# Performance work log

Measured on AMD Instinct MI355X. Metric: run time of the kernel, lower is better.

## Reference

```python
import jax, jax.numpy as jnp
import numpy as np
from jax import lax

B, T, N, C, AD, HW, KS, KT = 32, 8, 196, 768, 192, 14, 3, 3
EPS = 1e-5

def _groupnorm1(x, gamma, beta, axes):
    # GroupNorm(1, C): normalize over channel+spatial dims per sample
    mu = jnp.mean(x, axis=axes, keepdims=True)
    var = jnp.mean((x - mu) ** 2, axis=axes, keepdims=True)
    xn = (x - mu) * lax.rsqrt(var + EPS)
    shape = [1] * x.ndim
    shape[1] = -1
    return xn * gamma.reshape(shape) + beta.reshape(shape)

def setup_inputs() -> dict:
    key = jax.random.key(0)
    ks = jax.random.split(key, 16)
    s = 0.02
    return {
        'x': jax.random.normal(ks[0], (B, T, N + 1, C), jnp.float32),
        'w_down': jax.random.normal(ks[1], (C, AD), jnp.float32) * s,
        'b_down': jnp.zeros((AD,), jnp.float32),
        'w_sdw': jax.random.normal(ks[2], (AD, 1, KS, KS), jnp.float32) * s,
        'w_spw': jax.random.normal(ks[3], (AD, AD), jnp.float32) * s,  # [out,in]
        'g_snorm': jnp.ones((AD,), jnp.float32),
        'b_snorm': jnp.zeros((AD,), jnp.float32),
        'w_diff': jax.random.normal(ks[4], (AD, AD), jnp.float32) * s,  # [in,out]
        'w_tdw': jax.random.normal(ks[5], (AD, 1, KT), jnp.float32) * s,
        'w_tpw': jax.random.normal(ks[6], (AD, AD), jnp.float32) * s,  # [out,in]
        'g_tnorm': jnp.ones((AD,), jnp.float32),
        'b_tnorm': jnp.zeros((AD,), jnp.float32),
        'w_g1': jax.random.normal(ks[7], (AD, AD), jnp.float32) * s,
        'b_g1': jnp.zeros((AD,), jnp.float32),
        'w_g2': jax.random.normal(ks[8], (AD, AD), jnp.float32) * s,
        'b_g2': jnp.zeros((AD,), jnp.float32),
        'w_up': jax.random.normal(ks[9], (AD, C), jnp.float32) * s,  # torch zero-inits; randomized for nontrivial test
        'b_up': jnp.zeros((C,), jnp.float32),
        'w_cls': jax.random.normal(ks[10], (AD, C), jnp.float32) * s,
        'b_cls': jnp.zeros((C,), jnp.float32),
    }

def reference(x, w_down, b_down, w_sdw, w_spw, g_snorm, b_snorm, w_diff,
              w_tdw, w_tpw, g_tnorm, b_tnorm, w_g1, b_g1, w_g2, b_g2,
              w_up, b_up, w_cls, b_cls):
    gelu = lambda v: jax.nn.gelu(v, approximate=False)  # torch nn.GELU default (erf)
    cls_token = x[:, :, :1, :]
    patch = x[:, :, 1:, :]
    b, t, n, _ = patch.shape
    hw = HW
    ph = patch @ w_down + b_down  # [b,t,n,ad]
    ad = ph.shape[-1]
    # spatial path: (b t) c h w
    sp = ph.reshape(b * t, hw, hw, ad).transpose(0, 3, 1, 2)
    sp = lax.conv_general_dilated(sp, w_sdw, (1, 1), 'SAME',
                                  feature_group_count=ad,
                                  dimension_numbers=('NCHW', 'OIHW', 'NCHW'))
    sp = _groupnorm1(sp, g_snorm, b_snorm, axes=(1, 2, 3))
    sp = gelu(sp)
    sp = jnp.einsum('bchw,oc->bohw', sp, w_spw)
    spatial = sp.transpose(0, 2, 3, 1).reshape(b, t, n, ad)
    # diff gating
    diff = jnp.concatenate([jnp.zeros_like(ph[:, :1]), ph[:, 1:] - ph[:, :-1]], axis=1)
    diff = diff + diff @ w_diff
    # temporal path: (b n) c t
    tp = (ph + diff).transpose(0, 2, 3, 1).reshape(b * n, ad, t)
    tp = lax.conv_general_dilated(tp, w_tdw, (1,), 'SAME',
                                  feature_group_count=ad,
                                  dimension_numbers=('NCH', 'OIH', 'NCH'))
    tp = _groupnorm1(tp, g_tnorm, b_tnorm, axes=(1, 2))
    tp = gelu(tp)
    tp = jnp.einsum('bct,oc->bot', tp, w_tpw)
    temporal = tp.reshape(b, n, ad, t).transpose(0, 3, 1, 2)
    # gate
    gi = jnp.mean(jnp.abs(diff), axis=(1, 2))  # [b, ad]
    gate = jax.nn.sigmoid(gelu(gi @ w_g1 + b_g1) @ w_g2 + b_g2)[:, None, None, :]
    fused = gate * temporal + (1.0 - gate) * spatial
    patch_out = patch + fused @ w_up + b_up
    cls_ctx = jnp.mean(fused, axis=2, keepdims=True)
    cls_out = cls_token + cls_ctx @ w_cls + b_cls
    return jnp.concatenate([cls_out, patch_out], axis=2)
```

## Files before the change

### kernel.cpp

```cpp
#include <hip/hip_runtime.h>
#include <hip/hip_bf16.h>
#include <math.h>

typedef __attribute__((ext_vector_type(8))) short s8v;
typedef __attribute__((ext_vector_type(4))) float f4v;

#define GN_EPS 1e-5f

__device__ __forceinline__ float s2f(short s) {
    unsigned int u = ((unsigned int)(unsigned short)s) << 16;
    float f; __builtin_memcpy(&f, &u, 4); return f;
}
__device__ __forceinline__ short f2s(float f) {
    __hip_bfloat16 h = __float2bfloat16(f);
    short s; __builtin_memcpy(&s, &h, 2); return s;
}
__device__ __forceinline__ float gelu_f(float x) {
    return 0.5f * x * (1.0f + erff(x * 0.7071067811865476f));
}
__device__ __forceinline__ void gload16(const void* g, void* l) {
    __builtin_amdgcn_global_load_lds((const __attribute__((address_space(1))) void*)g,
                                     (__attribute__((address_space(3))) void*)l,
                                     16, 0, 0);
}

__global__ void detect_kernel(const unsigned int* g_snorm_raw, int* flag) {
    if (threadIdx.x == 0) flag[0] = (g_snorm_raw[0] == 0x3F800000u) ? 1 : 0;
}

struct ConvArgs {
    const void* src[19];
    int cum[20];
};
__global__ __launch_bounds__(256)
void convert_kernel(ConvArgs a, short* __restrict__ dst, const int* __restrict__ dflag,
                    int total) {
    const int dt = dflag[0];
    int idx = blockIdx.x * 256 + threadIdx.x;
    const int stride = gridDim.x * 256;
    for (; idx < total; idx += stride) {
        int seg = 0;
        while (idx >= a.cum[seg + 1]) seg++;
        const int off = idx - a.cum[seg];
        const float v = dt ? ((const float*)a.src[seg])[off]
                           : s2f(((const short*)a.src[seg])[off]);
        dst[idx] = f2s(v);
    }
}

__global__ __launch_bounds__(256)
void transpose_kernel(const short* __restrict__ src, short* __restrict__ dst,
                      int R, int C) {
    const int idx = blockIdx.x * 256 + threadIdx.x;
    if (idx < R * C) {
        const int r = idx / C, c = idx - r * C;
        dst[c * R + r] = src[idx];
    }
}


#define AMAP_PLAIN 0
#define AMAP_X     1
#define AMAP_DIFF  2
#define EPI_BIASH 0
#define EPI_H     1
#define EPI_DIFF  2
#define EPI_UP    3

template<int K_DIM, int N_DIM, int AMAP, int EPI>
__global__ __launch_bounds__(256)
void gemm_kernel(const void* __restrict__ Asrc, const short* __restrict__ Bmat,
                 const short* __restrict__ bias, const short* __restrict__ phH,
                 const void* __restrict__ xExt, short* __restrict__ outH,
                 void* __restrict__ outExt, const int* __restrict__ dflag)
{
    const int dt = dflag[0];

    __shared__ short As[2][2048];
    __shared__ short Bs[2][2048];

    const int tid  = threadIdx.x;
    const int lane = tid & 63;
    const int wave = tid >> 6;
    const int wr = wave >> 1, wc = wave & 1;
    const int m16 = lane & 15, q = lane >> 4;
    const int rowBase = blockIdx.x * 64;
    const int colBase = blockIdx.y * 64;

    const int sr = tid >> 2;
    const int ss = tid & 3;
    const int sg = ss ^ ((sr >> 1) & 3);
    const int wOff = wave * 512;

    const int agrow = rowBase + sr;
    long aBase;
    int abt7 = 0;
    if constexpr (AMAP == AMAP_X) {
        const int bt = agrow / 196;
        aBase = (long)(agrow + bt + 1) * 768 + sg * 8;
    } else if constexpr (AMAP == AMAP_DIFF) {
        aBase = (long)agrow * K_DIM + sg * 8;
        abt7 = (agrow / 196) & 7;
    } else {
        aBase = (long)agrow * K_DIM + sg * 8;
    }
    const long bBase = (long)(colBase + sr) * K_DIM + sg * 8;

    const int ra = wr * 32 + m16;
    const int rb = wc * 32 + m16;
    const int oA0 = ra * 32 + (q ^ ((ra >> 1) & 3)) * 8;
    const int oB0 = rb * 32 + (q ^ ((rb >> 1) & 3)) * 8;
    const int oA1 = oA0 + 512;
    const int oB1 = oB0 + 512;

    f4v acc[2][2] = {};
    constexpr int NK = K_DIM / 32;

    auto stage = [&](int kk, int buf) {
        if constexpr (AMAP == AMAP_PLAIN) {
            gload16((const short*)Asrc + aBase + kk, (void*)&As[buf][wOff]);
        } else if constexpr (AMAP == AMAP_X) {
            if (dt) {
                const float* xp = (const float*)Asrc + aBase + kk;
                const float4 f0 = *(const float4*)xp;
                const float4 f1 = *(const float4*)(xp + 4);
                s8v av;
                av[0] = f2s(f0.x); av[1] = f2s(f0.y); av[2] = f2s(f0.z); av[3] = f2s(f0.w);
                av[4] = f2s(f1.x); av[5] = f2s(f1.y); av[6] = f2s(f1.z); av[7] = f2s(f1.w);
                *(s8v*)&As[buf][sr * 32 + ss * 8] = av;
            } else {
                gload16((const short*)Asrc + aBase + kk, (void*)&As[buf][wOff]);
            }
        } else {
            s8v av;
            if (abt7) {
                const short* p1 = (const short*)Asrc + aBase + kk;
                const s8v v1 = *(const s8v*)p1;
                const s8v v0 = *(const s8v*)(p1 - 37632);
                #pragma unroll
                for (int j = 0; j < 8; j++) av[j] = f2s(s2f(v1[j]) - s2f(v0[j]));
            } else {
                #pragma unroll
                for (int j = 0; j < 8; j++) av[j] = 0;
            }
            *(s8v*)&As[buf][sr * 32 + ss * 8] = av;
        }
        gload16(Bmat + bBase + kk, (void*)&Bs[buf][wOff]);
    };

    stage(0, 0);
    __syncthreads();

    int cur = 0;
    for (int t = 0; t < NK; ++t) {
        if (t + 1 < NK) stage((t + 1) * 32, cur ^ 1);

        const s8v afr0 = *(const s8v*)&As[cur][oA0];
        const s8v afr1 = *(const s8v*)&As[cur][oA1];
        const s8v bfr0 = *(const s8v*)&Bs[cur][oB0];
        const s8v bfr1 = *(const s8v*)&Bs[cur][oB1];

        acc[0][0] = __builtin_amdgcn_mfma_f32_16x16x32_bf16(afr0, bfr0, acc[0][0], 0, 0, 0);
        acc[0][1] = __builtin_amdgcn_mfma_f32_16x16x32_bf16(afr0, bfr1, acc[0][1], 0, 0, 0);
        acc[1][0] = __builtin_amdgcn_mfma_f32_16x16x32_bf16(afr1, bfr0, acc[1][0], 0, 0, 0);
        acc[1][1] = __builtin_amdgcn_mfma_f32_16x16x32_bf16(afr1, bfr1, acc[1][1], 0, 0, 0);

        __syncthreads();
        cur ^= 1;
    }

    #pragma unroll
    for (int i = 0; i < 2; i++) {
        #pragma unroll
        for (int r = 0; r < 4; r++) {
            const int grow = rowBase + wr * 32 + i * 16 + q * 4 + r;
            #pragma unroll
            for (int j = 0; j < 2; j++) {
                const int gc = colBase + wc * 32 + j * 16 + m16;
                float v = acc[i][j][r];
                if constexpr (EPI == EPI_BIASH) {
                    outH[(long)grow * N_DIM + gc] = f2s(v + s2f(bias[gc]));
                } else if constexpr (EPI == EPI_H) {
                    outH[(long)grow * N_DIM + gc] = f2s(v);
                } else if constexpr (EPI == EPI_DIFF) {
                    const int bt = grow / 196;
                    const int t = bt & 7;
                    const float phv = s2f(phH[(long)grow * 192 + gc]);
                    float d = (t > 0) ? (phv - s2f(phH[(long)(grow - 196) * 192 + gc])) : 0.0f;
                    outH[(long)grow * 192 + gc] = f2s(v + phv + d);
                } else {
                    const int bt = grow / 196;
                    const long oi = (long)(grow + bt + 1) * 768 + gc;
                    const float bv = v + s2f(bias[gc]);
                    if (dt) {
                        ((float*)outExt)[oi] = ((const float*)xExt)[oi] + bv;
                    } else {
                        ((short*)outExt)[oi] = f2s(s2f(((const short*)xExt)[oi]) + bv);
                    }
                }
            }
        }
    }
}

__global__ __launch_bounds__(1024, 4)
void spatial_kernel(const short* __restrict__ ph, const short* __restrict__ w_sdw,
                    const short* __restrict__ g_s, const short* __restrict__ b_s,
                    short* __restrict__ snorm)
{
    __shared__ short tile[196 * 192];
    __shared__ short wkT[9 * 192];
    __shared__ float gsl[192], bsl[192];
    __shared__ float redA[16], redB[16];
    __shared__ float stats[2];

    const int bt = blockIdx.x, tid = threadIdx.x;
    const short* Pg = ph + (long)bt * 37632;

    for (int i = tid; i < 4704; i += 1024)
        *(s8v*)&tile[i * 8] = *(const s8v*)&Pg[i * 8];
    for (int i = tid; i < 1728; i += 1024) {
        const int c = i / 9, tap = i - c * 9;
        wkT[tap * 192 + c] = w_sdw[i];
    }
    if (tid < 192) { gsl[tid] = s2f(g_s[tid]); bsl[tid] = s2f(b_s[tid]); }
    __syncthreads();

    float val[5][8];
    float lsum = 0.f, lsq = 0.f;
    #pragma unroll
    for (int it = 0; it < 5; it++) {
        const int i = tid + it * 1024;
        #pragma unroll
        for (int k = 0; k < 8; k++) val[it][k] = 0.f;
        if (i < 4704) {
            const int n = i / 24, c8 = i - n * 24;
            const int h = n / 14, w = n - (n / 14) * 14;
            float a[8] = {0.f,0.f,0.f,0.f,0.f,0.f,0.f,0.f};
            #pragma unroll
            for (int tap = 0; tap < 9; tap++) {
                const int dh = tap / 3 - 1, dw = tap % 3 - 1;
                const int hh = h + dh, ww = w + dw;
                if (hh >= 0 && hh < 14 && ww >= 0 && ww < 14) {
                    s8v iv = *(const s8v*)&tile[(hh * 14 + ww) * 192 + c8 * 8];
                    s8v wv = *(const s8v*)&wkT[tap * 192 + c8 * 8];
                    #pragma unroll
                    for (int k = 0; k < 8; k++) a[k] += s2f(iv[k]) * s2f(wv[k]);
                }
            }
            #pragma unroll
            for (int k = 0; k < 8; k++) {
                val[it][k] = a[k]; lsum += a[k]; lsq += a[k] * a[k];
            }
        }
    }
    #pragma unroll
    for (int d = 1; d < 64; d <<= 1) {
        lsum += __shfl_xor(lsum, d, 64);
        lsq  += __shfl_xor(lsq,  d, 64);
    }
    if ((tid & 63) == 0) { redA[tid >> 6] = lsum; redB[tid >> 6] = lsq; }
    __syncthreads();
    if (tid < 64) {
        float s = (tid < 16) ? redA[tid] : 0.f;
        float qq = (tid < 16) ? redB[tid] : 0.f;
        #pragma unroll
        for (int d = 1; d < 16; d <<= 1) {
            s  += __shfl_xor(s,  d, 64);
            qq += __shfl_xor(qq, d, 64);
        }
        if (tid == 0) {
            const float inv = 1.0f / 37632.0f;
            const float mean = s * inv;
            const float var  = qq * inv - mean * mean;
            stats[0] = mean; stats[1] = rsqrtf(var + GN_EPS);
        }
    }
    __syncthreads();
    const float mean = stats[0], rstd = stats[1];
    short* Og = snorm + (long)bt * 37632;
    #pragma unroll
    for (int it = 0; it < 5; it++) {
        const int i = tid + it * 1024;
        if (i < 4704) {
            const int c8 = i - (i / 24) * 24;
            s8v o;
            #pragma unroll
            for (int k = 0; k < 8; k++) {
                const int c = c8 * 8 + k;
                const float y = (val[it][k] - mean) * rstd * gsl[c] + bsl[c];
                o[k] = f2s(gelu_f(y));
            }
            *(s8v*)&Og[i * 8] = o;
        }
    }
}

__global__ __launch_bounds__(192)
void gi_kernel(const short* __restrict__ tp, const short* __restrict__ ph,
               float* __restrict__ gi)
{
    const int bt = blockIdx.x;
    const int b = bt >> 3;
    const int tid = threadIdx.x;
    const int c8 = tid >> 3, sub = tid & 7;
    float part[8] = {0.f,0.f,0.f,0.f,0.f,0.f,0.f,0.f};
    for (int n = sub; n < 196; n += 8) {
        const long off = ((long)bt * 196 + n) * 192 + c8 * 8;
        s8v a = *(const s8v*)(tp + off);
        s8v p = *(const s8v*)(ph + off);
        #pragma unroll
        for (int k = 0; k < 8; k++) part[k] += fabsf(s2f(a[k]) - s2f(p[k]));
    }
    #pragma unroll
    for (int d = 1; d < 8; d <<= 1) {
        #pragma unroll
        for (int k = 0; k < 8; k++) part[k] += __shfl_xor(part[k], d, 64);
    }
    if (sub == 0) {
        #pragma unroll
        for (int k = 0; k < 8; k++) atomicAdd(&gi[b * 192 + c8 * 8 + k], part[k]);
    }
}

__global__ __launch_bounds__(192)
void temporal_kernel(const short* __restrict__ tp, const short* __restrict__ w_tdw,
                     const short* __restrict__ g_t, const short* __restrict__ b_t,
                     short* __restrict__ tnorm)
{
    const int bn = blockIdx.x;
    const int c = threadIdx.x;
    const int b = bn / 196, n = bn - (bn / 196) * 196;
    const long base = ((long)b * 8 * 196 + n) * 192 + c;
    const long ts = 196 * 192;
    float v[8], o[8];
    #pragma unroll
    for (int t = 0; t < 8; t++) v[t] = s2f(tp[base + t * ts]);
    const float w0 = s2f(w_tdw[c * 3]), w1 = s2f(w_tdw[c * 3 + 1]), w2 = s2f(w_tdw[c * 3 + 2]);
    #pragma unroll
    for (int t = 0; t < 8; t++) {
        float a = v[t] * w1;
        if (t > 0) a += v[t - 1] * w0;
        if (t < 7) a += v[t + 1] * w2;
        o[t] = a;
    }
    float lsum = 0.f, lsq = 0.f;
    #pragma unroll
    for (int t = 0; t < 8; t++) { lsum += o[t]; lsq += o[t] * o[t]; }
    __shared__ float red1[192], red2[192];
    red1[c] = lsum; red2[c] = lsq;
    __syncthreads();
    for (int s = 96; s > 2; s >>= 1) {
        if (c < s) { red1[c] += red1[c + s]; red2[c] += red2[c + s]; }
        __syncthreads();
    }
    const float mean = (red1[0] + red1[1] + red1[2]) * (1.0f / 1536.0f);
    const float var  = (red2[0] + red2[1] + red2[2]) * (1.0f / 1536.0f) - mean * mean;
    const float rstd = rsqrtf(var + GN_EPS);
    const float gg = s2f(g_t[c]), bb = s2f(b_t[c]);
    #pragma unroll
    for (int t = 0; t < 8; t++) {
        const float y = (o[t] - mean) * rstd * gg + bb;
        tnorm[base + t * ts] = f2s(gelu_f(y));
    }
}

__global__ __launch_bounds__(192)
void gate_kernel(const float* __restrict__ gi, const short* __restrict__ w_g1,
                 const short* __restrict__ b_g1, const short* __restrict__ w_g2,
                 const short* __restrict__ b_g2, float* __restrict__ gate)
{
    const int b = blockIdx.x, o = threadIdx.x;
    __shared__ float s0[192], s1[192];
    s0[o] = gi[b * 192 + o] * (1.0f / 1568.0f);
    __syncthreads();
    float a = s2f(b_g1[o]);
    for (int cc = 0; cc < 192; cc++) a += s0[cc] * s2f(w_g1[cc * 192 + o]);
    s1[o] = gelu_f(a);
    __syncthreads();
    float a2 = s2f(b_g2[o]);
    for (int cc = 0; cc < 192; cc++) a2 += s1[cc] * s2f(w_g2[cc * 192 + o]);
    gate[b * 192 + o] = 1.0f / (1.0f + expf(-a2));
}

__global__ __launch_bounds__(192)
void fuse_kernel(const short* __restrict__ temporal, const short* __restrict__ spatial,
                 const float* __restrict__ gate, short* __restrict__ fused,
                 float* __restrict__ cls_sum)
{
    const int bt = blockIdx.x;
    const int b = bt >> 3;
    const int tid = threadIdx.x;
    const int c8 = tid >> 3, sub = tid & 7;
    float g[8];
    {
        const float4* gp = (const float4*)&gate[b * 192 + c8 * 8];
        float4 ga = gp[0], gb = gp[1];
        g[0]=ga.x; g[1]=ga.y; g[2]=ga.z; g[3]=ga.w;
        g[4]=gb.x; g[5]=gb.y; g[6]=gb.z; g[7]=gb.w;
    }
    float part[8] = {0.f,0.f,0.f,0.f,0.f,0.f,0.f,0.f};
    for (int n = sub; n < 196; n += 8) {
        const long off = ((long)bt * 196 + n) * 192 + c8 * 8;
        s8v tv = *(const s8v*)(temporal + off);
        s8v sv = *(const s8v*)(spatial + off);
        s8v fv;
        #pragma unroll
        for (int k = 0; k < 8; k++) {
            const float f = g[k] * s2f(tv[k]) + (1.0f - g[k]) * s2f(sv[k]);
            fv[k] = f2s(f);
            part[k] += f;
        }
        *(s8v*)(fused + off) = fv;
    }
    #pragma unroll
    for (int d = 1; d < 8; d <<= 1) {
        #pragma unroll
        for (int k = 0; k < 8; k++) part[k] += __shfl_xor(part[k], d, 64);
    }
    if (sub == 0) {
        #pragma unroll
        for (int k = 0; k < 8; k++)
            cls_sum[bt * 192 + c8 * 8 + k] = part[k] * (1.0f / 196.0f);
    }
}

__global__ __launch_bounds__(256)
void cls_kernel(const float* __restrict__ cls_sum, const short* __restrict__ w_cls,
                const short* __restrict__ b_cls, const void* __restrict__ x,
                void* __restrict__ out, const int* __restrict__ dflag)
{
    const int dt = dflag[0];
    const int bt = blockIdx.x, tid = threadIdx.x;
    __shared__ float ctx[192];
    if (tid < 192) ctx[tid] = cls_sum[bt * 192 + tid];
    __syncthreads();
    for (int oc = tid; oc < 768; oc += 256) {
        float a = s2f(b_cls[oc]);
        for (int cc = 0; cc < 192; cc++) a += ctx[cc] * s2f(w_cls[cc * 768 + oc]);
        const long oi = (long)bt * 197 * 768 + oc;
        if (dt) ((float*)out)[oi] = ((const float*)x)[oi] + a;
        else    ((short*)out)[oi] = f2s(s2f(((const short*)x)[oi]) + a);
    }
}

extern "C" void kernel_launch(void* const* d_in, const int* in_sizes, int n_in,
                              void* d_out, int out_size, void* d_ws, size_t ws_size,
                              hipStream_t stream) {
    const void* x = d_in[0];

    const long F = 50176L * 192L;
    short* wsS = (short*)d_ws;
    short* P = wsS;
    short* Q = wsS + F;
    short* R = wsS + 2 * F;
    short* S = wsS + 3 * F;
    short* W = wsS + 4 * F;
    int cum[20]; cum[0] = 0;
    for (int i = 1; i <= 19; i++) cum[i] = cum[i - 1] + in_sizes[i];
    const int totalW = cum[19];

    short* WT   = W + ((totalW + 7) & ~7);
    short* wdT  = WT;
    short* wdfT = WT + 147456;
    short* wupT = WT + 147456 + 36864;

    float* smalls = (float*)(WT + 331776);
    float* gi      = smalls;
    float* gate    = smalls + 6144;
    float* cls_sum = smalls + 12288;
    int*   dflag   = (int*)(smalls + 61440);

    const short* b_down = W + cum[1];
    const short* w_sdw  = W + cum[2];
    const short* w_spw  = W + cum[3];
    const short* g_sn   = W + cum[4];
    const short* b_sn   = W + cum[5];
    const short* w_tdw  = W + cum[7];
    const short* w_tpw  = W + cum[8];
    const short* g_tn   = W + cum[9];
    const short* b_tn   = W + cum[10];
    const short* w_g1   = W + cum[11];
    const short* b_g1   = W + cum[12];
    const short* w_g2   = W + cum[13];
    const short* b_g2   = W + cum[14];
    const short* b_up   = W + cum[16];
    const short* w_cls  = W + cum[17];
    const short* b_cls  = W + cum[18];

    hipMemsetAsync(gi, 0, 6144 * sizeof(float), stream);
    detect_kernel<<<1, 64, 0, stream>>>((const unsigned int*)d_in[5], dflag);

    ConvArgs ca;
    for (int i = 0; i < 19; i++) ca.src[i] = d_in[i + 1];
    for (int i = 0; i < 20; i++) ca.cum[i] = cum[i];
    convert_kernel<<<618, 256, 0, stream>>>(ca, W, dflag, totalW);

    transpose_kernel<<<576, 256, 0, stream>>>(W + cum[0],  wdT,  768, 192);
    transpose_kernel<<<144, 256, 0, stream>>>(W + cum[6],  wdfT, 192, 192);
    transpose_kernel<<<576, 256, 0, stream>>>(W + cum[15], wupT, 192, 768);

    dim3 g3(784, 3), g12(784, 12);

    gemm_kernel<768, 192, AMAP_X, EPI_BIASH>
        <<<g3, 256, 0, stream>>>(x, wdT, b_down, nullptr, nullptr, P, nullptr, dflag);
    spatial_kernel<<<256, 1024, 0, stream>>>(P, w_sdw, g_sn, b_sn, R);
    gemm_kernel<192, 192, AMAP_PLAIN, EPI_H>
        <<<g3, 256, 0, stream>>>(R, w_spw, nullptr, nullptr, nullptr, S, nullptr, dflag);
    gemm_kernel<192, 192, AMAP_DIFF, EPI_DIFF>
        <<<g3, 256, 0, stream>>>(P, wdfT, nullptr, P, nullptr, Q, nullptr, dflag);
    gi_kernel<<<256, 192, 0, stream>>>(Q, P, gi);
    temporal_kernel<<<6272, 192, 0, stream>>>(Q, w_tdw, g_tn, b_tn, R);
    gemm_kernel<192, 192, AMAP_PLAIN, EPI_H>
        <<<g3, 256, 0, stream>>>(R, w_tpw, nullptr, nullptr, nullptr, Q, nullptr, dflag);
    gate_kernel<<<32, 192, 0, stream>>>(gi, w_g1, b_g1, w_g2, b_g2, gate);
    fuse_kernel<<<256, 192, 0, stream>>>(Q, S, gate, R, cls_sum);
    gemm_kernel<192, 768, AMAP_PLAIN, EPI_UP>
        <<<g12, 256, 0, stream>>>(R, wupT, b_up, nullptr, x, nullptr, d_out, dflag);
    cls_kernel<<<256, 256, 0, stream>>>(cls_sum, w_cls, b_cls, x, d_out, dflag);
}
```

Measured before the change: 607.4 us.

## Transpose MFMA output for vectorized epilogue stores and fuse gate-input reduction into diff GEMM

Swaps the MFMA operand order so each lane holds four consecutive columns of one row. This lets every GEMM epilogue use 4-wide vector loads and stores instead of scalar ones. The diff GEMM epilogue now also computes |diff| and reduces it across rows with shuffles before atomically adding into the gate input. This removes the separate gi_kernel pass that reread Q and P. The trade-offs are extra shuffle and atomic work inside the GEMM epilogue, and the abs values now come from fp32 before bf16 rounding.

```diff
diff --git a/kernel.cpp b/kernel.cpp
--- a/kernel.cpp
+++ b/kernel.cpp
@@ -3,6 +3,7 @@
 #include <math.h>
 
 typedef __attribute__((ext_vector_type(8))) short s8v;
+typedef __attribute__((ext_vector_type(4))) short s4v;
 typedef __attribute__((ext_vector_type(4))) float f4v;
 
 #define GN_EPS 1e-5f
@@ -72,7 +73,8 @@
 void gemm_kernel(const void* __restrict__ Asrc, const short* __restrict__ Bmat,
                  const short* __restrict__ bias, const short* __restrict__ phH,
                  const void* __restrict__ xExt, short* __restrict__ outH,
-                 void* __restrict__ outExt, const int* __restrict__ dflag)
+                 void* __restrict__ outExt, float* __restrict__ giOut,
+                 const int* __restrict__ dflag)
 {
     const int dt = dflag[0];
 
@@ -160,10 +162,10 @@
         const s8v bfr0 = *(const s8v*)&Bs[cur][oB0];
         const s8v bfr1 = *(const s8v*)&Bs[cur][oB1];
 
-        acc[0][0] = __builtin_amdgcn_mfma_f32_16x16x32_bf16(afr0, bfr0, acc[0][0], 0, 0, 0);
-        acc[0][1] = __builtin_amdgcn_mfma_f32_16x16x32_bf16(afr0, bfr1, acc[0][1], 0, 0, 0);
-        acc[1][0] = __builtin_amdgcn_mfma_f32_16x16x32_bf16(afr1, bfr0, acc[1][0], 0, 0, 0);
-        acc[1][1] = __builtin_amdgcn_mfma_f32_16x16x32_bf16(afr1, bfr1, acc[1][1], 0, 0, 0);
+        acc[0][0] = __builtin_amdgcn_mfma_f32_16x16x32_bf16(bfr0, afr0, acc[0][0], 0, 0, 0);
+        acc[0][1] = __builtin_amdgcn_mfma_f32_16x16x32_bf16(bfr1, afr0, acc[0][1], 0, 0, 0);
+        acc[1][0] = __builtin_amdgcn_mfma_f32_16x16x32_bf16(bfr0, afr1, acc[1][0], 0, 0, 0);
+        acc[1][1] = __builtin_amdgcn_mfma_f32_16x16x32_bf16(bfr1, afr1, acc[1][1], 0, 0, 0);
 
         __syncthreads();
         cur ^= 1;
@@ -171,32 +173,84 @@
 
     #pragma unroll
     for (int i = 0; i < 2; i++) {
-        #pragma unroll
-        for (int r = 0; r < 4; r++) {
-            const int grow = rowBase + wr * 32 + i * 16 + q * 4 + r;
+        const int grow = rowBase + wr * 32 + i * 16 + m16;
+        const int gcb  = colBase + wc * 32 + q * 4;
+
+        if constexpr (EPI == EPI_BIASH) {
             #pragma unroll
             for (int j = 0; j < 2; j++) {
-                const int gc = colBase + wc * 32 + j * 16 + m16;
-                float v = acc[i][j][r];
-                if constexpr (EPI == EPI_BIASH) {
-                    outH[(long)grow * N_DIM + gc] = f2s(v + s2f(bias[gc]));
-                } else if constexpr (EPI == EPI_H) {
-                    outH[(long)grow * N_DIM + gc] = f2s(v);
-                } else if constexpr (EPI == EPI_DIFF) {
-                    const int bt = grow / 196;
-                    const int t = bt & 7;
-                    const float phv = s2f(phH[(long)grow * 192 + gc]);
-                    float d = (t > 0) ? (phv - s2f(phH[(long)(grow - 196) * 192 + gc])) : 0.0f;
-                    outH[(long)grow * 192 + gc] = f2s(v + phv + d);
+                const int gc = gcb + j * 16;
+                const s4v bv = *(const s4v*)&bias[gc];
+                s4v o;
+                #pragma unroll
+                for (int r = 0; r < 4; r++) o[r] = f2s(acc[i][j][r] + s2f(bv[r]));
+                *(s4v*)&outH[(long)grow * N_DIM + gc] = o;
+            }
+        } else if constexpr (EPI == EPI_H) {
+            #pragma unroll
+            for (int j = 0; j < 2; j++) {
+                const int gc = gcb + j * 16;
+                s4v o;
+                #pragma unroll
+                for (int r = 0; r < 4; r++) o[r] = f2s(acc[i][j][r]);
+                *(s4v*)&outH[(long)grow * N_DIM + gc] = o;
+            }
+        } else if constexpr (EPI == EPI_DIFF) {
+            const int t = (grow / 196) & 7;
+            float ga[8];
+            #pragma unroll
+            for (int j = 0; j < 2; j++) {
+                const int gc = gcb + j * 16;
+                const long pOff = (long)grow * 192 + gc;
+                const s4v p1 = *(const s4v*)&phH[pOff];
+                s4v p0 = p1;
+                if (t > 0) p0 = *(const s4v*)&phH[pOff - 37632];
+                s4v o;
+                #pragma unroll
+                for (int r = 0; r < 4; r++) {
+                    const float phv = s2f(p1[r]);
+                    const float d = (t > 0) ? (phv - s2f(p0[r])) : 0.0f;
+                    const float tpmp = acc[i][j][r] + d;
+                    ga[j * 4 + r] = fabsf(tpmp);
+                    o[r] = f2s(tpmp + phv);
+                }
+                *(s4v*)&outH[pOff] = o;
+            }
+            #pragma unroll
+            for (int mlt = 1; mlt < 16; mlt <<= 1) {
+                #pragma unroll
+                for (int k = 0; k < 8; k++) ga[k] += __shfl_xor(ga[k], mlt, 64);
+            }
+            if (m16 == 0) {
+                const int b = (rowBase + wr * 32 + i * 16) / 1568;
+                #pragma unroll
+                for (int k = 0; k < 8; k++) {
+                    const int col = colBase + wc * 32 + (k >> 2) * 16 + q * 4 + (k & 3);
+                    atomicAdd(&giOut[b * 192 + col], ga[k]);
+                }
+            }
+        } else {
+            const int bt = grow / 196;
+            const long orow = (long)(grow + bt + 1) * 768;
+            #pragma unroll
+            for (int j = 0; j < 2; j++) {
+                const int gc = gcb + j * 16;
+                const s4v bv = *(const s4v*)&bias[gc];
+                if (dt) {
+                    const float4 xv = *(const float4*)((const float*)xExt + orow + gc);
+                    float4 ov;
+                    ov.x = xv.x + acc[i][j][0] + s2f(bv[0]);
+                    ov.y = xv.y + acc[i][j][1] + s2f(bv[1]);
+                    ov.z = xv.z + acc[i][j][2] + s2f(bv[2]);
+                    ov.w = xv.w + acc[i][j][3] + s2f(bv[3]);
+                    *(float4*)((float*)outExt + orow + gc) = ov;
                 } else {
-                    const int bt = grow / 196;
-                    const long oi = (long)(grow + bt + 1) * 768 + gc;
-                    const float bv = v + s2f(bias[gc]);
-                    if (dt) {
-                        ((float*)outExt)[oi] = ((const float*)xExt)[oi] + bv;
-                    } else {
-                        ((short*)outExt)[oi] = f2s(s2f(((const short*)xExt)[oi]) + bv);
-                    }
+                    const s4v xv = *(const s4v*)((const short*)xExt + orow + gc);
+                    s4v ov;
+                    #pragma unroll
+                    for (int r = 0; r < 4; r++)
+                        ov[r] = f2s(s2f(xv[r]) + acc[i][j][r] + s2f(bv[r]));
+                    *(s4v*)((short*)outExt + orow + gc) = ov;
                 }
             }
         }
@@ -293,33 +347,6 @@
             }
             *(s8v*)&Og[i * 8] = o;
         }
-    }
-}
-
-__global__ __launch_bounds__(192)
-void gi_kernel(const short* __restrict__ tp, const short* __restrict__ ph,
-               float* __restrict__ gi)
-{
-    const int bt = blockIdx.x;
-    const int b = bt >> 3;
-    const int tid = threadIdx.x;
-    const int c8 = tid >> 3, sub = tid & 7;
-    float part[8] = {0.f,0.f,0.f,0.f,0.f,0.f,0.f,0.f};
-    for (int n = sub; n < 196; n += 8) {
-        const long off = ((long)bt * 196 + n) * 192 + c8 * 8;
-        s8v a = *(const s8v*)(tp + off);
-        s8v p = *(const s8v*)(ph + off);
-        #pragma unroll
-        for (int k = 0; k < 8; k++) part[k] += fabsf(s2f(a[k]) - s2f(p[k]));
-    }
-    #pragma unroll
-    for (int d = 1; d < 8; d <<= 1) {
-        #pragma unroll
-        for (int k = 0; k < 8; k++) part[k] += __shfl_xor(part[k], d, 64);
-    }
-    if (sub == 0) {
-        #pragma unroll
-        for (int k = 0; k < 8; k++) atomicAdd(&gi[b * 192 + c8 * 8 + k], part[k]);
     }
 }
 
@@ -503,19 +530,18 @@
     dim3 g3(784, 3), g12(784, 12);
 
     gemm_kernel<768, 192, AMAP_X, EPI_BIASH>
-        <<<g3, 256, 0, stream>>>(x, wdT, b_down, nullptr, nullptr, P, nullptr, dflag);
+        <<<g3, 256, 0, stream>>>(x, wdT, b_down, nullptr, nullptr, P, nullptr, nullptr, dflag);
     spatial_kernel<<<256, 1024, 0, stream>>>(P, w_sdw, g_sn, b_sn, R);
     gemm_kernel<192, 192, AMAP_PLAIN, EPI_H>
-        <<<g3, 256, 0, stream>>>(R, w_spw, nullptr, nullptr, nullptr, S, nullptr, dflag);
+        <<<g3, 256, 0, stream>>>(R, w_spw, nullptr, nullptr, nullptr, S, nullptr, nullptr, dflag);
     gemm_kernel<192, 192, AMAP_DIFF, EPI_DIFF>
-        <<<g3, 256, 0, stream>>>(P, wdfT, nullptr, P, nullptr, Q, nullptr, dflag);
-    gi_kernel<<<256, 192, 0, stream>>>(Q, P, gi);
+        <<<g3, 256, 0, stream>>>(P, wdfT, nullptr, P, nullptr, Q, nullptr, gi, dflag);
     temporal_kernel<<<6272, 192, 0, stream>>>(Q, w_tdw, g_tn, b_tn, R);
     gemm_kernel<192, 192, AMAP_PLAIN, EPI_H>
-        <<<g3, 256, 0, stream>>>(R, w_tpw, nullptr, nullptr, nullptr, Q, nullptr, dflag);
+        <<<g3, 256, 0, stream>>>(R, w_tpw, nullptr, nullptr, nullptr, Q, nullptr, nullptr, dflag);
     gate_kernel<<<32, 192, 0, stream>>>(gi, w_g1, b_g1, w_g2, b_g2, gate);
     fuse_kernel<<<256, 192, 0, stream>>>(Q, S, gate, R, cls_sum);
     gemm_kernel<192, 768, AMAP_PLAIN, EPI_UP>
-        <<<g12, 256, 0, stream>>>(R, wupT, b_up, nullptr, x, nullptr, d_out, dflag);
+        <<<g12, 256, 0, stream>>>(R, wupT, b_up, nullptr, x, nullptr, d_out, nullptr, dflag);
     cls_kernel<<<256, 256, 0, stream>>>(cls_sum, w_cls, b_cls, x, d_out, dflag);
 }
```

Result: slower. 620.5 us (+2.2%).
